# Kernel tuning notes

Measured on AMD Instinct MI355X. Metric: run time of the kernel, lower is better.

Reference implementation:

```python
import jax, jax.numpy as jnp
import numpy as np

N_QUBITS = 20
W_MUL = (2.0 ** 0.5) * (5.0 ** -0.5)  # he_std = gain * 5**-0.5, use_wscale=True, lrmul=1

_C = jnp.complex64
X = jnp.array([[0, 1], [1, 0]], dtype=_C)
Y = jnp.array([[0, -1j], [1j, 0]], dtype=_C)
Z = jnp.array([[1, 0], [0, -1]], dtype=_C)
I2 = jnp.eye(2, dtype=_C)
I4 = jnp.eye(4, dtype=_C)
XX = jnp.kron(X, X)
YY = jnp.kron(Y, Y)
ZZ = jnp.kron(Z, Z)


def _rot(theta, pauli, ident):
    # exp(-i * theta/2 * P) = cos(theta/2) I - i sin(theta/2) P
    a = theta * 0.5
    return jnp.cos(a) * ident - (1j * jnp.sin(a)) * pauli


def _apply_1q(state, g, w):
    # state: [batch] + [2]*n ; contract gate input index with qubit axis w
    s = jnp.tensordot(g, state, axes=((1,), (w + 1,)))
    return jnp.moveaxis(s, 0, w + 1)


def _apply_2q(state, g4, w0, w1):
    g = g4.reshape(2, 2, 2, 2)  # (out0, out1, in0, in1)
    s = jnp.tensordot(g, state, axes=((2, 3), (w0 + 1, w1 + 1)))
    return jnp.moveaxis(s, (0, 1), (w0 + 1, w1 + 1))


def _xyz_layer(psi, params, n):
    # params: [3n]; rx, ry, rz on each wire
    for q in range(n):
        psi = _apply_1q(psi, _rot(params[3 * q], X, I2), q)
        psi = _apply_1q(psi, _rot(params[3 * q + 1], Y, I2), q)
        psi = _apply_1q(psi, _rot(params[3 * q + 2], Z, I2), q)
    return psi


def _circuit(psi, w, n):
    psi = _xyz_layer(psi, w[: 3 * n], n)
    for q in range(n - 1):
        i = 3 * n + 3 * q
        psi = _apply_2q(psi, _rot(w[i], XX, I4), q, q + 1)
        psi = _apply_2q(psi, _rot(w[i + 1], YY, I4), q, q + 1)
        psi = _apply_2q(psi, _rot(w[i + 2], ZZ, I4), q, q + 1)
    psi = _xyz_layer(psi, w[6 * n - 3 :], n)
    return psi


def setup_inputs() -> dict:
    key = jax.random.key(0)
    k1, k2 = jax.random.split(key)
    n = N_QUBITS
    dim = 1 << n
    batch = 4
    x = jax.random.normal(k1, (batch, 1, dim), dtype=jnp.float32)
    weight = jax.random.uniform(k2, (9 * n - 3,), dtype=jnp.float32, minval=0.0, maxval=2.0 * np.pi)
    return {"x": x, "weight": weight, "dimA": 10}


def reference(x, weight, dimA):
    n = N_QUBITS
    batch = x.shape[0]
    w = weight * W_MUL
    psi = x.astype(_C).reshape((batch,) + (2,) * n)  # MPS tensor [b, 2, ..., 2]
    psi = _circuit(psi, w, n)
    dimB = n - dimA
    # partial trace of |psi><psi| over the first dimB qubits (most-significant axes):
    # reduced[a, c] = sum_t psi[t, a] * conj(psi[t, c])  -- never materialize the full DM
    psi = psi.reshape(batch, 1 << dimB, 1 << dimA)
    rdm = jnp.einsum('bta,btc->bac', psi, psi.conj())
    # return real/imag stacked on last axis (real-valued representation of complex DM)
    return jnp.stack([rdm.real, rdm.imag], axis=-1)
```

## Files before the change

kernel.cpp:

```cpp
#include <hip/hip_runtime.h>
#include <hip/hip_bf16.h>

#define N_Q    20
#define DIM    (1 << N_Q)
#define BATCH  4
#define NGATES 19
#define L2OFF  117

typedef float2 c32;
typedef __attribute__((ext_vector_type(8))) short short8;
typedef __attribute__((ext_vector_type(4))) float f32x4;
typedef __attribute__((ext_vector_type(4))) unsigned int u32x4;

__device__ __forceinline__ c32 cmul(c32 a, c32 b) {
    return make_float2(fmaf(a.x, b.x, -a.y * b.y), fmaf(a.x, b.y, a.y * b.x));
}
__device__ __forceinline__ c32 cmadd(c32 acc, c32 a, c32 b) {
    acc.x = fmaf(a.x, b.x, fmaf(-a.y, b.y, acc.x));
    acc.y = fmaf(a.x, b.y, fmaf(a.y, b.x, acc.y));
    return acc;
}
__device__ __forceinline__ unsigned short f2bf(float f) {
    union { float f; unsigned u; } v; v.f = f;
    unsigned r = v.u + 0x7FFFu + ((v.u >> 16) & 1u);
    return (unsigned short)(r >> 16);
}
__device__ __forceinline__ void gll16(const void* g, void* l) {
    __builtin_amdgcn_global_load_lds((const __attribute__((address_space(1))) void*)g,
                                     (__attribute__((address_space(3))) void*)l, 16, 0, 0);
}

__device__ void mm2(const c32 A[2][2], const c32 B[2][2], c32 C[2][2]) {
    for (int i = 0; i < 2; i++)
        for (int j = 0; j < 2; j++) {
            c32 s = make_float2(0.f, 0.f);
            for (int k = 0; k < 2; k++) s = cmadd(s, A[i][k], B[k][j]);
            C[i][j] = s;
        }
}
__device__ void mm4(const c32 A[4][4], const c32 B[4][4], c32 C[4][4]) {
    for (int i = 0; i < 4; i++)
        for (int j = 0; j < 4; j++) {
            c32 s = make_float2(0.f, 0.f);
            for (int k = 0; k < 4; k++) s = cmadd(s, A[i][k], B[k][j]);
            C[i][j] = s;
        }
}
__device__ void single_u(const float* w, int base, c32 U[2][2]) {
    const float WM = 0.63245553203367586640f;
    float hx = w[base] * WM * 0.5f, hy = w[base + 1] * WM * 0.5f, hz = w[base + 2] * WM * 0.5f;
    float cx = cosf(hx), sx = sinf(hx);
    float cy = cosf(hy), sy = sinf(hy);
    float cz = cosf(hz), sz = sinf(hz);
    c32 RX[2][2] = {{{cx, 0.f}, {0.f, -sx}}, {{0.f, -sx}, {cx, 0.f}}};
    c32 RY[2][2] = {{{cy, 0.f}, {-sy, 0.f}}, {{sy, 0.f}, {cy, 0.f}}};
    c32 RZ[2][2] = {{{cz, -sz}, {0.f, 0.f}}, {{0.f, 0.f}, {cz, sz}}};
    c32 T[2][2];
    mm2(RY, RX, T);
    mm2(RZ, T, U);
}
__device__ void kron22(const c32 A[2][2], const c32 B[2][2], c32 K[4][4]) {
    for (int i = 0; i < 2; i++)
        for (int j = 0; j < 2; j++)
            for (int k = 0; k < 2; k++)
                for (int l = 0; l < 2; l++)
                    K[i * 2 + j][k * 2 + l] = cmul(A[i][k], B[j][l]);
}

__global__ void build_gates(const float* __restrict__ w, c32* __restrict__ G) {
    int q = threadIdx.x;
    if (q >= NGATES) return;
    const float WM = 0.63245553203367586640f;
    float hx = w[60 + 3 * q] * WM * 0.5f;
    float hy = w[61 + 3 * q] * WM * 0.5f;
    float hz = w[62 + 3 * q] * WM * 0.5f;
    float cx = cosf(hx), sx = sinf(hx);
    float cy = cosf(hy), sy = sinf(hy);
    float cz = cosf(hz), sz = sinf(hz);
    c32 RXX[4][4], RYY[4][4], RZZ[4][4];
    for (int i = 0; i < 4; i++)
        for (int j = 0; j < 4; j++) {
            RXX[i][j] = make_float2(0.f, 0.f);
            RYY[i][j] = make_float2(0.f, 0.f);
            RZZ[i][j] = make_float2(0.f, 0.f);
        }
    for (int i = 0; i < 4; i++) {
        RXX[i][i]     = make_float2(cx, 0.f);
        RXX[i][3 - i] = make_float2(0.f, -sx);
        RYY[i][i]     = make_float2(cy, 0.f);
    }
    RYY[0][3] = make_float2(0.f,  sy);
    RYY[1][2] = make_float2(0.f, -sy);
    RYY[2][1] = make_float2(0.f, -sy);
    RYY[3][0] = make_float2(0.f,  sy);
    RZZ[0][0] = make_float2(cz, -sz);
    RZZ[1][1] = make_float2(cz,  sz);
    RZZ[2][2] = make_float2(cz,  sz);
    RZZ[3][3] = make_float2(cz, -sz);
    c32 T[4][4], M[4][4];
    mm4(RYY, RXX, T);
    mm4(RZZ, T, M);

    c32 I2m[2][2] = {{{1.f, 0.f}, {0.f, 0.f}}, {{0.f, 0.f}, {1.f, 0.f}}};
    c32 Ua[2][2], Ub[2][2], Pre[4][4], Post[4][4];
    if (q == 0) {
        single_u(w, 0, Ua);
        single_u(w, 3, Ub);
        kron22(Ua, Ub, Pre);
    } else {
        single_u(w, 3 * (q + 1), Ub);
        kron22(I2m, Ub, Pre);
    }
    if (q == NGATES - 1) {
        single_u(w, L2OFF + 3 * 18, Ua);
        single_u(w, L2OFF + 3 * 19, Ub);
        kron22(Ua, Ub, Post);
    } else {
        single_u(w, L2OFF + 3 * q, Ua);
        kron22(Ua, I2m, Post);
    }
    c32 T2[4][4], Gq[4][4];
    mm4(M, Pre, T2);
    mm4(Post, T2, Gq);
    for (int i = 0; i < 4; i++)
        for (int j = 0; j < 4; j++)
            G[q * 16 + i * 4 + j] = Gq[i][j];
}

__device__ __forceinline__ void apply4(const c32* g, c32& x0, c32& x1, c32& x2, c32& x3) {
    c32 r0 = cmul(g[0],  x0); r0 = cmadd(r0, g[1],  x1); r0 = cmadd(r0, g[2],  x2); r0 = cmadd(r0, g[3],  x3);
    c32 r1 = cmul(g[4],  x0); r1 = cmadd(r1, g[5],  x1); r1 = cmadd(r1, g[6],  x2); r1 = cmadd(r1, g[7],  x3);
    c32 r2 = cmul(g[8],  x0); r2 = cmadd(r2, g[9],  x1); r2 = cmadd(r2, g[10], x2); r2 = cmadd(r2, g[11], x3);
    c32 r3 = cmul(g[12], x0); r3 = cmadd(r3, g[13], x1); r3 = cmadd(r3, g[14], x2); r3 = cmadd(r3, g[15], x3);
    x0 = r0; x1 = r1; x2 = r2; x3 = r3;
}
__device__ __forceinline__ void load_gate(const c32* __restrict__ gp, c32 g[16]) {
#pragma unroll
    for (int k = 0; k < 16; k++) g[k] = gp[k];
}
template <int LO>
__device__ __forceinline__ void gate_on32(c32 v[32], const c32 g[16]) {
#pragma unroll
    for (int m = 0; m < 8; ++m) {
        const int j0 = ((m >> LO) << (LO + 2)) | (m & ((1 << LO) - 1));
        const int s = 1 << LO;
        apply4(g, v[j0], v[j0 + s], v[j0 + 2 * s], v[j0 + 3 * s]);
    }
}
template <int LO>
__device__ __forceinline__ void gate_on16(c32* v, const c32 g[16]) {
#pragma unroll
    for (int m = 0; m < 4; ++m) {
        const int j0 = ((m >> LO) << (LO + 2)) | (m & ((1 << LO) - 1));
        const int s = 1 << LO;
        apply4(g, v[j0], v[j0 + s], v[j0 + 2 * s], v[j0 + 3 * s]);
    }
}

#define SIDX(l) ((l) ^ ((((l) >> 5) & 15)))

__global__ __launch_bounds__(256) void pass_a2(const float* __restrict__ x,
                                               c32* __restrict__ psi,
                                               const c32* __restrict__ Gall) {
    __shared__ __align__(16) char smem[65536];
    float* xs = (float*)smem;
    c32* s = (c32*)smem;
    int b = blockIdx.x >> 7;
    int c0 = (blockIdx.x & 127) << 5;
    const float* xp = x + ((size_t)b << 20) + c0;
    c32* pp = psi + ((size_t)b << 20) + c0;
    int t = threadIdx.x;
#pragma unroll
    for (int i = 0; i < 8; ++i) {
        int f4 = t + (i << 8);
        int row = f4 >> 3, sl = f4 & 7;
        float4 v = *reinterpret_cast<const float4*>(xp + (size_t)row * 4096 + sl * 4);
        reinterpret_cast<float4*>(xs)[row * 8 + (sl ^ (row & 7))] = v;
    }
    __syncthreads();
    int col = t & 31, rlow = t >> 5;
    c32 v[32], g[16];
#pragma unroll
    for (int j = 0; j < 32; ++j) {
        int row = (j << 3) | rlow;
        float re = xs[row * 32 + ((((col >> 2) ^ (row & 7)) << 2) | (col & 3))];
        v[j] = make_float2(re, 0.f);
    }
    __syncthreads();
    load_gate(Gall + 0 * 16, g);  gate_on32<3>(v, g);
    load_gate(Gall + 1 * 16, g);  gate_on32<2>(v, g);
    load_gate(Gall + 2 * 16, g);  gate_on32<1>(v, g);
    load_gate(Gall + 3 * 16, g);  gate_on32<0>(v, g);
#pragma unroll
    for (int j = 0; j < 32; ++j) {
        int l = ((((j << 3) | rlow) << 5)) | col;
        s[SIDX(l)] = v[j];
    }
    __syncthreads();
    int rhi = t >> 5;
#pragma unroll
    for (int rtop = 0; rtop < 2; ++rtop)
#pragma unroll
        for (int j = 0; j < 16; ++j) {
            int row = (rtop << 7) | (rhi << 4) | j;
            int l = (row << 5) | col;
            v[rtop * 16 + j] = s[SIDX(l)];
        }
    load_gate(Gall + 4 * 16, g);  gate_on16<2>(v, g);  gate_on16<2>(v + 16, g);
    load_gate(Gall + 5 * 16, g);  gate_on16<1>(v, g);  gate_on16<1>(v + 16, g);
    load_gate(Gall + 6 * 16, g);  gate_on16<0>(v, g);  gate_on16<0>(v + 16, g);
#pragma unroll
    for (int rtop = 0; rtop < 2; ++rtop)
#pragma unroll
        for (int j = 0; j < 16; ++j) {
            int row = (rtop << 7) | (rhi << 4) | j;
            pp[(size_t)row * 4096 + col] = v[rtop * 16 + j];
        }
}

__global__ __launch_bounds__(256) void pass_b2(const c32* __restrict__ psi,
                                               unsigned short* __restrict__ Brt,
                                               unsigned short* __restrict__ Bit,
                                               const c32* __restrict__ Gall) {
    __shared__ c32 s[8192];
    int b = blockIdx.x >> 7;
    int chunk = blockIdx.x & 127;
    const c32* pp = psi + ((size_t)b << 20) + ((size_t)chunk << 13);
    int t = threadIdx.x;
    c32 v[32], g[16];
#pragma unroll
    for (int j = 0; j < 32; ++j) v[j] = pp[(j << 8) | t];
    load_gate(Gall + 7 * 16, g);   gate_on32<3>(v, g);
    load_gate(Gall + 8 * 16, g);   gate_on32<2>(v, g);
    load_gate(Gall + 9 * 16, g);   gate_on32<1>(v, g);
    load_gate(Gall + 10 * 16, g);  gate_on32<0>(v, g);
#pragma unroll
    for (int j = 0; j < 32; ++j) { int l = (j << 8) | t; s[SIDX(l)] = v[j]; }
    __syncthreads();
    int hi2 = (t >> 4) << 9, lo2 = t & 15;
#pragma unroll
    for (int j = 0; j < 32; ++j) { int l = hi2 | (j << 4) | lo2; v[j] = s[SIDX(l)]; }
    load_gate(Gall + 11 * 16, g);  gate_on32<3>(v, g);
    load_gate(Gall + 12 * 16, g);  gate_on32<2>(v, g);
    load_gate(Gall + 13 * 16, g);  gate_on32<1>(v, g);
    load_gate(Gall + 14 * 16, g);  gate_on32<0>(v, g);
    __syncthreads();
#pragma unroll
    for (int j = 0; j < 32; ++j) { int l = hi2 | (j << 4) | lo2; s[SIDX(l)] = v[j]; }
    __syncthreads();
#pragma unroll
    for (int j = 0; j < 32; ++j) { int l = (t << 5) | j; v[j] = s[SIDX(l)]; }
    load_gate(Gall + 15 * 16, g);  gate_on32<3>(v, g);
    load_gate(Gall + 16 * 16, g);  gate_on32<2>(v, g);
    load_gate(Gall + 17 * 16, g);  gate_on32<1>(v, g);
    load_gate(Gall + 18 * 16, g);  gate_on32<0>(v, g);
    size_t off = ((size_t)b << 20) + ((size_t)chunk << 13) + ((size_t)t << 5);
#pragma unroll
    for (int p = 0; p < 4; ++p) {
        unsigned short rr[8], ri[8];
#pragma unroll
        for (int i = 0; i < 8; ++i) {
            rr[i] = f2bf(v[8 * p + i].x);
            ri[i] = f2bf(v[8 * p + i].y);
        }
        *reinterpret_cast<float4*>(Brt + off + 8 * p) = *reinterpret_cast<float4*>(rr);
        *reinterpret_cast<float4*>(Bit + off + 8 * p) = *reinterpret_cast<float4*>(ri);
    }
}

__global__ __launch_bounds__(256) void bt_t(const unsigned short* __restrict__ Brt,
                                            const unsigned short* __restrict__ Bit,
                                            unsigned short* __restrict__ Art,
                                            unsigned short* __restrict__ Ait) {
    __shared__ unsigned lds32[64 * 66];
    int b  = blockIdx.z;
    int t0 = blockIdx.x * 64;
    int a0 = blockIdx.y * 64;
    size_t gb = (size_t)b << 20;
#pragma unroll
    for (int h = 0; h < 2; ++h) {
        int p = threadIdx.x + h * 256;
        int r = p >> 3, cq = p & 7;
        size_t src = gb + (size_t)(t0 + r) * 1024 + a0 + cq * 8;
        float4 fr = *reinterpret_cast<const float4*>(Brt + src);
        float4 fi = *reinterpret_cast<const float4*>(Bit + src);
        const unsigned short* ur = reinterpret_cast<const unsigned short*>(&fr);
        const unsigned short* ui = reinterpret_cast<const unsigned short*>(&fi);
#pragma unroll
        for (int i = 0; i < 8; ++i)
            lds32[r * 66 + cq * 8 + i] = (unsigned)ur[i] | ((unsigned)ui[i] << 16);
    }
    __syncthreads();
#pragma unroll
    for (int h = 0; h < 2; ++h) {
        int q = threadIdx.x + h * 256;
        int a = q >> 3, tq = q & 7;
        unsigned short rr[8], ri[8];
#pragma unroll
        for (int i = 0; i < 8; ++i) {
            unsigned w = lds32[(tq * 8 + i) * 66 + a];
            rr[i] = (unsigned short)(w & 0xFFFF);
            ri[i] = (unsigned short)(w >> 16);
        }
        size_t dst = gb + (size_t)(a0 + a) * 1024 + t0 + tq * 8;
        *reinterpret_cast<float4*>(Art + dst) = *reinterpret_cast<float4*>(rr);
        *reinterpret_cast<float4*>(Ait + dst) = *reinterpret_cast<float4*>(ri);
    }
}

__global__ __launch_bounds__(512) void gram_mfma5b(const unsigned short* __restrict__ Art,
                                                   const unsigned short* __restrict__ Ait,
                                                   float2* __restrict__ out) {
    __shared__ __align__(16) unsigned short lds[2][4][8192];
    int hw = blockIdx.x;
    int virt = (hw & 7) * 18 + (hw >> 3);
    int b = virt / 36;
    int rem = virt - b * 36;
    int ia = 0;
    while (rem >= 8 - ia) { rem -= 8 - ia; ++ia; }
    int ic = ia + rem;
    int a0 = ia * 128, c0 = ic * 128;
    int tid = threadIdx.x;
    int lane = tid & 63, w = tid >> 6;
    int wm = w & 3, wn = w >> 2;
    int arr = w >> 1, half = w & 1;
    const unsigned short* sp = (arr & 1) ? Ait : Art;
    int prow = (arr < 2) ? a0 : c0;
    int srow = lane >> 3, sslot = lane & 7;
    size_t gb = (size_t)b << 20;

    f32x4 accRe[2][4], accIm[2][4];
#pragma unroll
    for (int m = 0; m < 2; m++)
#pragma unroll
        for (int n = 0; n < 4; n++) { accRe[m][n] = (f32x4)0.f; accIm[m][n] = (f32x4)0.f; }

#define STAGE5(KT, BUF)                                                                   \
    {                                                                                     \
        _Pragma("unroll")                                                                 \
        for (int i = 0; i < 8; ++i) {                                                     \
            int r = (half << 6) | (i << 3) | srow;                                        \
            int sl = sslot ^ srow;                                                        \
            const unsigned short* gp = sp + gb + ((size_t)(prow + r) << 10) + (KT) * 64 + sl * 8; \
            gll16(gp, &lds[BUF][arr][((half << 6) | (i << 3)) * 64 + lane * 8]);          \
        }                                                                                 \
    }

    STAGE5(0, 0);
    for (int kt = 0; kt < 16; ++kt) {
        int cur = kt & 1;
        if (kt < 15) {
            STAGE5(kt + 1, cur ^ 1);
            asm volatile("s_waitcnt vmcnt(8)" ::: "memory");
        } else {
            asm volatile("s_waitcnt vmcnt(0)" ::: "memory");
        }
        __builtin_amdgcn_s_barrier();
        __builtin_amdgcn_sched_barrier(0);
#pragma unroll
        for (int kk = 0; kk < 2; ++kk) {
            int sbase = kk * 4 + (lane >> 4);
            short8 am[2][2], bn[4][2];
#pragma unroll
            for (int m = 0; m < 2; m++) {
                int r = wm * 32 + m * 16 + (lane & 15);
                int off = r * 64 + ((sbase ^ (r & 7)) << 3);
                am[m][0] = *reinterpret_cast<const short8*>(&lds[cur][0][off]);
                am[m][1] = *reinterpret_cast<const short8*>(&lds[cur][1][off]);
            }
#pragma unroll
            for (int n = 0; n < 4; n++) {
                int r = wn * 64 + n * 16 + (lane & 15);
                int off = r * 64 + ((sbase ^ (r & 7)) << 3);
                bn[n][0] = *reinterpret_cast<const short8*>(&lds[cur][2][off]);
                bn[n][1] = *reinterpret_cast<const short8*>(&lds[cur][3][off]);
            }
#pragma unroll
            for (int m = 0; m < 2; m++) {
                u32x4 tn = *reinterpret_cast<u32x4*>(&am[m][0]) ^ 0x80008000u;
                short8 arn = *reinterpret_cast<short8*>(&tn);
#pragma unroll
                for (int n = 0; n < 4; n++) {
                    accRe[m][n] = __builtin_amdgcn_mfma_f32_16x16x32_bf16(am[m][0], bn[n][0], accRe[m][n], 0, 0, 0);
                    accRe[m][n] = __builtin_amdgcn_mfma_f32_16x16x32_bf16(am[m][1], bn[n][1], accRe[m][n], 0, 0, 0);
                    accIm[m][n] = __builtin_amdgcn_mfma_f32_16x16x32_bf16(am[m][1], bn[n][0], accIm[m][n], 0, 0, 0);
                    accIm[m][n] = __builtin_amdgcn_mfma_f32_16x16x32_bf16(arn,      bn[n][1], accIm[m][n], 0, 0, 0);
                }
            }
        }
        asm volatile("s_waitcnt lgkmcnt(0)" ::: "memory");
        __builtin_amdgcn_sched_barrier(0);
        __builtin_amdgcn_s_barrier();
        __builtin_amdgcn_sched_barrier(0);
    }
#undef STAGE5
    size_t ob = gb;
#pragma unroll
    for (int m = 0; m < 2; m++)
#pragma unroll
        for (int n = 0; n < 4; n++)
#pragma unroll
            for (int r = 0; r < 4; r++) {
                int a = a0 + wm * 32 + m * 16 + (lane >> 4) * 4 + r;
                int c = c0 + wn * 64 + n * 16 + (lane & 15);
                out[ob + ((size_t)a << 10) + c] = make_float2(accRe[m][n][r], accIm[m][n][r]);
            }
    if (ia != ic) {
        float2* mlds = reinterpret_cast<float2*>(&lds[0][0][0]);
#pragma unroll
        for (int h = 0; h < 2; ++h) {
            __syncthreads();
            if (wn == h) {
#pragma unroll
                for (int m = 0; m < 2; m++)
#pragma unroll
                    for (int n = 0; n < 4; n++)
#pragma unroll
                        for (int r = 0; r < 4; r++) {
                            int a_l = wm * 32 + m * 16 + (lane >> 4) * 4 + r;
                            int c_l = n * 16 + (lane & 15);
                            mlds[c_l * 131 + a_l] = make_float2(accRe[m][n][r], -accIm[m][n][r]);
                        }
            }
            __syncthreads();
#pragma unroll
            for (int i = 0; i < 16; ++i) {
                int p = tid + (i << 9);
                int row = p >> 7, col = p & 127;
                out[ob + ((size_t)(c0 + h * 64 + row) << 10) + a0 + col] = mlds[row * 131 + col];
            }
        }
    }
}

extern "C" void kernel_launch(void* const* d_in, const int* in_sizes, int n_in,
                              void* d_out, int out_size, void* d_ws, size_t ws_size,
                              hipStream_t stream) {
    const float* x = (const float*)d_in[0];
    const float* weight = (const float*)d_in[1];
    const size_t psiBytes = (size_t)BATCH * DIM * sizeof(c32);
    c32* psi = (c32*)d_ws;
    c32* G = (c32*)((char*)d_ws + psiBytes);
    unsigned short* Brt = (unsigned short*)((char*)d_ws + psiBytes + 65536);
    unsigned short* Bit = Brt + (size_t)BATCH * DIM;
    unsigned short* Art = Bit + (size_t)BATCH * DIM;
    unsigned short* Ait = Art + (size_t)BATCH * DIM;

    build_gates<<<1, 64, 0, stream>>>(weight, G);
    pass_a2<<<BATCH * 128, 256, 0, stream>>>(x, psi, G);
    pass_b2<<<BATCH * 128, 256, 0, stream>>>(psi, Brt, Bit, G);
    bt_t<<<dim3(16, 16, BATCH), 256, 0, stream>>>(Brt, Bit, Art, Ait);
    gram_mfma5b<<<144, 512, 0, stream>>>(Art, Ait, (float2*)d_out);
}
```

Measured before the change: 101.2 us.

## Use packed-float gate application and restructure gram prefetch pipeline with priority

```diff
diff --git a/kernel.cpp b/kernel.cpp
--- a/kernel.cpp
+++ b/kernel.cpp
@@ -6,8 +6,10 @@
 #define BATCH  4
 #define NGATES 19
 #define L2OFF  117
+#define GSTRIDE 32
 
 typedef float2 c32;
+typedef __attribute__((ext_vector_type(2))) float fv2;
 typedef __attribute__((ext_vector_type(8))) short short8;
 typedef __attribute__((ext_vector_type(4))) float f32x4;
 typedef __attribute__((ext_vector_type(4))) unsigned int u32x4;
@@ -123,37 +125,49 @@
     mm4(M, Pre, T2);
     mm4(Post, T2, Gq);
     for (int i = 0; i < 4; i++)
-        for (int j = 0; j < 4; j++)
-            G[q * 16 + i * 4 + j] = Gq[i][j];
-}
-
-__device__ __forceinline__ void apply4(const c32* g, c32& x0, c32& x1, c32& x2, c32& x3) {
-    c32 r0 = cmul(g[0],  x0); r0 = cmadd(r0, g[1],  x1); r0 = cmadd(r0, g[2],  x2); r0 = cmadd(r0, g[3],  x3);
-    c32 r1 = cmul(g[4],  x0); r1 = cmadd(r1, g[5],  x1); r1 = cmadd(r1, g[6],  x2); r1 = cmadd(r1, g[7],  x3);
-    c32 r2 = cmul(g[8],  x0); r2 = cmadd(r2, g[9],  x1); r2 = cmadd(r2, g[10], x2); r2 = cmadd(r2, g[11], x3);
-    c32 r3 = cmul(g[12], x0); r3 = cmadd(r3, g[13], x1); r3 = cmadd(r3, g[14], x2); r3 = cmadd(r3, g[15], x3);
+        for (int j = 0; j < 4; j++) {
+            c32 g = Gq[i][j];
+            G[q * GSTRIDE + i * 4 + j]      = g;
+            G[q * GSTRIDE + 16 + i * 4 + j] = make_float2(-g.y, g.x);
+        }
+}
+
+__device__ __forceinline__ void apply4pk(const fv2 g[16], const fv2 gs[16],
+                                         fv2& x0, fv2& x1, fv2& x2, fv2& x3) {
+    fv2 a0 = (fv2)(x0[0]), b0 = (fv2)(x0[1]);
+    fv2 a1 = (fv2)(x1[0]), b1 = (fv2)(x1[1]);
+    fv2 a2 = (fv2)(x2[0]), b2 = (fv2)(x2[1]);
+    fv2 a3 = (fv2)(x3[0]), b3 = (fv2)(x3[1]);
+    fv2 r0 = a0 * g[0];  r0 += b0 * gs[0];  r0 += a1 * g[1];  r0 += b1 * gs[1];
+    r0 += a2 * g[2];     r0 += b2 * gs[2];  r0 += a3 * g[3];  r0 += b3 * gs[3];
+    fv2 r1 = a0 * g[4];  r1 += b0 * gs[4];  r1 += a1 * g[5];  r1 += b1 * gs[5];
+    r1 += a2 * g[6];     r1 += b2 * gs[6];  r1 += a3 * g[7];  r1 += b3 * gs[7];
+    fv2 r2 = a0 * g[8];  r2 += b0 * gs[8];  r2 += a1 * g[9];  r2 += b1 * gs[9];
+    r2 += a2 * g[10];    r2 += b2 * gs[10]; r2 += a3 * g[11]; r2 += b3 * gs[11];
+    fv2 r3 = a0 * g[12]; r3 += b0 * gs[12]; r3 += a1 * g[13]; r3 += b1 * gs[13];
+    r3 += a2 * g[14];    r3 += b2 * gs[14]; r3 += a3 * g[15]; r3 += b3 * gs[15];
     x0 = r0; x1 = r1; x2 = r2; x3 = r3;
 }
-__device__ __forceinline__ void load_gate(const c32* __restrict__ gp, c32 g[16]) {
-#pragma unroll
-    for (int k = 0; k < 16; k++) g[k] = gp[k];
+__device__ __forceinline__ void load_gate2(const fv2* __restrict__ gp, fv2 g[16], fv2 gs[16]) {
+#pragma unroll
+    for (int k = 0; k < 16; k++) { g[k] = gp[k]; gs[k] = gp[16 + k]; }
 }
 template <int LO>
-__device__ __forceinline__ void gate_on32(c32 v[32], const c32 g[16]) {
+__device__ __forceinline__ void gate_on32(fv2 v[32], const fv2 g[16], const fv2 gs[16]) {
 #pragma unroll
     for (int m = 0; m < 8; ++m) {
         const int j0 = ((m >> LO) << (LO + 2)) | (m & ((1 << LO) - 1));
         const int s = 1 << LO;
-        apply4(g, v[j0], v[j0 + s], v[j0 + 2 * s], v[j0 + 3 * s]);
+        apply4pk(g, gs, v[j0], v[j0 + s], v[j0 + 2 * s], v[j0 + 3 * s]);
     }
 }
 template <int LO>
-__device__ __forceinline__ void gate_on16(c32* v, const c32 g[16]) {
+__device__ __forceinline__ void gate_on16(fv2* v, const fv2 g[16], const fv2 gs[16]) {
 #pragma unroll
     for (int m = 0; m < 4; ++m) {
         const int j0 = ((m >> LO) << (LO + 2)) | (m & ((1 << LO) - 1));
         const int s = 1 << LO;
-        apply4(g, v[j0], v[j0 + s], v[j0 + 2 * s], v[j0 + 3 * s]);
+        apply4pk(g, gs, v[j0], v[j0 + s], v[j0 + 2 * s], v[j0 + 3 * s]);
     }
 }
 
@@ -164,11 +178,12 @@
                                                const c32* __restrict__ Gall) {
     __shared__ __align__(16) char smem[65536];
     float* xs = (float*)smem;
-    c32* s = (c32*)smem;
+    fv2* s = (fv2*)smem;
+    const fv2* Gf = (const fv2*)Gall;
     int b = blockIdx.x >> 7;
     int c0 = (blockIdx.x & 127) << 5;
     const float* xp = x + ((size_t)b << 20) + c0;
-    c32* pp = psi + ((size_t)b << 20) + c0;
+    fv2* pp = (fv2*)(psi + ((size_t)b << 20) + c0);
     int t = threadIdx.x;
 #pragma unroll
     for (int i = 0; i < 8; ++i) {
@@ -179,18 +194,18 @@
     }
     __syncthreads();
     int col = t & 31, rlow = t >> 5;
-    c32 v[32], g[16];
+    fv2 v[32], g[16], gs[16];
 #pragma unroll
     for (int j = 0; j < 32; ++j) {
         int row = (j << 3) | rlow;
         float re = xs[row * 32 + ((((col >> 2) ^ (row & 7)) << 2) | (col & 3))];
-        v[j] = make_float2(re, 0.f);
-    }
-    __syncthreads();
-    load_gate(Gall + 0 * 16, g);  gate_on32<3>(v, g);
-    load_gate(Gall + 1 * 16, g);  gate_on32<2>(v, g);
-    load_gate(Gall + 2 * 16, g);  gate_on32<1>(v, g);
-    load_gate(Gall + 3 * 16, g);  gate_on32<0>(v, g);
+        v[j] = (fv2){re, 0.f};
+    }
+    __syncthreads();
+    load_gate2(Gf + 0 * GSTRIDE, g, gs);  gate_on32<3>(v, g, gs);
+    load_gate2(Gf + 1 * GSTRIDE, g, gs);  gate_on32<2>(v, g, gs);
+    load_gate2(Gf + 2 * GSTRIDE, g, gs);  gate_on32<1>(v, g, gs);
+    load_gate2(Gf + 3 * GSTRIDE, g, gs);  gate_on32<0>(v, g, gs);
 #pragma unroll
     for (int j = 0; j < 32; ++j) {
         int l = ((((j << 3) | rlow) << 5)) | col;
@@ -206,9 +221,9 @@
             int l = (row << 5) | col;
             v[rtop * 16 + j] = s[SIDX(l)];
         }
-    load_gate(Gall + 4 * 16, g);  gate_on16<2>(v, g);  gate_on16<2>(v + 16, g);
-    load_gate(Gall + 5 * 16, g);  gate_on16<1>(v, g);  gate_on16<1>(v + 16, g);
-    load_gate(Gall + 6 * 16, g);  gate_on16<0>(v, g);  gate_on16<0>(v + 16, g);
+    load_gate2(Gf + 4 * GSTRIDE, g, gs);  gate_on16<2>(v, g, gs);  gate_on16<2>(v + 16, g, gs);
+    load_gate2(Gf + 5 * GSTRIDE, g, gs);  gate_on16<1>(v, g, gs);  gate_on16<1>(v + 16, g, gs);
+    load_gate2(Gf + 6 * GSTRIDE, g, gs);  gate_on16<0>(v, g, gs);  gate_on16<0>(v + 16, g, gs);
 #pragma unroll
     for (int rtop = 0; rtop < 2; ++rtop)
 #pragma unroll
@@ -222,46 +237,47 @@
                                                unsigned short* __restrict__ Brt,
                                                unsigned short* __restrict__ Bit,
                                                const c32* __restrict__ Gall) {
-    __shared__ c32 s[8192];
+    __shared__ fv2 s[8192];
+    const fv2* Gf = (const fv2*)Gall;
     int b = blockIdx.x >> 7;
     int chunk = blockIdx.x & 127;
-    const c32* pp = psi + ((size_t)b << 20) + ((size_t)chunk << 13);
+    const fv2* pp = (const fv2*)(psi + ((size_t)b << 20) + ((size_t)chunk << 13));
     int t = threadIdx.x;
-    c32 v[32], g[16];
+    fv2 v[32], g[16], gs[16];
 #pragma unroll
     for (int j = 0; j < 32; ++j) v[j] = pp[(j << 8) | t];
-    load_gate(Gall + 7 * 16, g);   gate_on32<3>(v, g);
-    load_gate(Gall + 8 * 16, g);   gate_on32<2>(v, g);
-    load_gate(Gall + 9 * 16, g);   gate_on32<1>(v, g);
-    load_gate(Gall + 10 * 16, g);  gate_on32<0>(v, g);
+    load_gate2(Gf + 7 * GSTRIDE, g, gs);   gate_on32<3>(v, g, gs);
+    load_gate2(Gf + 8 * GSTRIDE, g, gs);   gate_on32<2>(v, g, gs);
+    load_gate2(Gf + 9 * GSTRIDE, g, gs);   gate_on32<1>(v, g, gs);
+    load_gate2(Gf + 10 * GSTRIDE, g, gs);  gate_on32<0>(v, g, gs);
 #pragma unroll
     for (int j = 0; j < 32; ++j) { int l = (j << 8) | t; s[SIDX(l)] = v[j]; }
     __syncthreads();
     int hi2 = (t >> 4) << 9, lo2 = t & 15;
 #pragma unroll
     for (int j = 0; j < 32; ++j) { int l = hi2 | (j << 4) | lo2; v[j] = s[SIDX(l)]; }
-    load_gate(Gall + 11 * 16, g);  gate_on32<3>(v, g);
-    load_gate(Gall + 12 * 16, g);  gate_on32<2>(v, g);
-    load_gate(Gall + 13 * 16, g);  gate_on32<1>(v, g);
-    load_gate(Gall + 14 * 16, g);  gate_on32<0>(v, g);
+    load_gate2(Gf + 11 * GSTRIDE, g, gs);  gate_on32<3>(v, g, gs);
+    load_gate2(Gf + 12 * GSTRIDE, g, gs);  gate_on32<2>(v, g, gs);
+    load_gate2(Gf + 13 * GSTRIDE, g, gs);  gate_on32<1>(v, g, gs);
+    load_gate2(Gf + 14 * GSTRIDE, g, gs);  gate_on32<0>(v, g, gs);
     __syncthreads();
 #pragma unroll
     for (int j = 0; j < 32; ++j) { int l = hi2 | (j << 4) | lo2; s[SIDX(l)] = v[j]; }
     __syncthreads();
 #pragma unroll
     for (int j = 0; j < 32; ++j) { int l = (t << 5) | j; v[j] = s[SIDX(l)]; }
-    load_gate(Gall + 15 * 16, g);  gate_on32<3>(v, g);
-    load_gate(Gall + 16 * 16, g);  gate_on32<2>(v, g);
-    load_gate(Gall + 17 * 16, g);  gate_on32<1>(v, g);
-    load_gate(Gall + 18 * 16, g);  gate_on32<0>(v, g);
+    load_gate2(Gf + 15 * GSTRIDE, g, gs);  gate_on32<3>(v, g, gs);
+    load_gate2(Gf + 16 * GSTRIDE, g, gs);  gate_on32<2>(v, g, gs);
+    load_gate2(Gf + 17 * GSTRIDE, g, gs);  gate_on32<1>(v, g, gs);
+    load_gate2(Gf + 18 * GSTRIDE, g, gs);  gate_on32<0>(v, g, gs);
     size_t off = ((size_t)b << 20) + ((size_t)chunk << 13) + ((size_t)t << 5);
 #pragma unroll
     for (int p = 0; p < 4; ++p) {
         unsigned short rr[8], ri[8];
 #pragma unroll
         for (int i = 0; i < 8; ++i) {
-            rr[i] = f2bf(v[8 * p + i].x);
-            ri[i] = f2bf(v[8 * p + i].y);
+            rr[i] = f2bf(v[8 * p + i][0]);
+            ri[i] = f2bf(v[8 * p + i][1]);
         }
         *reinterpret_cast<float4*>(Brt + off + 8 * p) = *reinterpret_cast<float4*>(rr);
         *reinterpret_cast<float4*>(Bit + off + 8 * p) = *reinterpret_cast<float4*>(ri);
@@ -308,7 +324,7 @@
     }
 }
 
-__global__ __launch_bounds__(512) void gram_mfma5b(const unsigned short* __restrict__ Art,
+__global__ __launch_bounds__(512) void gram_mfma5c(const unsigned short* __restrict__ Art,
                                                    const unsigned short* __restrict__ Ait,
                                                    float2* __restrict__ out) {
     __shared__ __align__(16) unsigned short lds[2][4][8192];
@@ -349,14 +365,11 @@
     STAGE5(0, 0);
     for (int kt = 0; kt < 16; ++kt) {
         int cur = kt & 1;
-        if (kt < 15) {
-            STAGE5(kt + 1, cur ^ 1);
-            asm volatile("s_waitcnt vmcnt(8)" ::: "memory");
-        } else {
-            asm volatile("s_waitcnt vmcnt(0)" ::: "memory");
-        }
+        asm volatile("s_waitcnt vmcnt(0)" ::: "memory");
         __builtin_amdgcn_s_barrier();
         __builtin_amdgcn_sched_barrier(0);
+        if (kt < 15) STAGE5(kt + 1, cur ^ 1);
+        __builtin_amdgcn_s_setprio(1);
 #pragma unroll
         for (int kk = 0; kk < 2; ++kk) {
             int sbase = kk * 4 + (lane >> 4);
@@ -388,9 +401,8 @@
                 }
             }
         }
+        __builtin_amdgcn_s_setprio(0);
         asm volatile("s_waitcnt lgkmcnt(0)" ::: "memory");
-        __builtin_amdgcn_sched_barrier(0);
-        __builtin_amdgcn_s_barrier();
         __builtin_amdgcn_sched_barrier(0);
     }
 #undef STAGE5
@@ -450,5 +462,5 @@
     pass_a2<<<BATCH * 128, 256, 0, stream>>>(x, psi, G);
     pass_b2<<<BATCH * 128, 256, 0, stream>>>(psi, Brt, Bit, G);
     bt_t<<<dim3(16, 16, BATCH), 256, 0, stream>>>(Brt, Bit, Art, Ait);
-    gram_mfma5b<<<144, 512, 0, stream>>>(Art, Ait, (float2*)d_out);
-}
+    gram_mfma5c<<<144, 512, 0, stream>>>(Art, Ait, (float2*)d_out);
+}
```

Measured after the change: 101.1 us. About the same (-0.1%).
